# Kernel tuning notes

Hardware: AMD Instinct MI355X
Metric: run time of the kernel (lower is better)

## Reference

```python
import jax, jax.numpy as jnp
import numpy as np


def setup_inputs() -> dict:
    key = jax.random.key(0)
    k1, k2, k3, k4 = jax.random.split(key, 4)
    B, T, D, HS = 4, 2048, 1024, 64
    x = jax.random.normal(k1, (B, T, D), dtype=jnp.float32)
    # nn.Linear(d_model, head_size, bias=False) weights: (head_size, d_model)
    s = 1.0 / np.sqrt(D)
    Wk = jax.random.normal(k2, (HS, D), dtype=jnp.float32) * s
    Wq = jax.random.normal(k3, (HS, D), dtype=jnp.float32) * s
    Wv = jax.random.normal(k4, (HS, D), dtype=jnp.float32) * s
    return {"x": x, "Wk": Wk, "Wq": Wq, "Wv": Wv}


def reference(x, Wk, Wq, Wv):
    # x: [B, T, D]; W*: [HS, D]
    B, T, D = x.shape
    HS = Wk.shape[0]
    k = jnp.einsum('btd,hd->bth', x, Wk)  # [B, T, HS]
    q = jnp.einsum('btd,hd->bth', x, Wq)
    v = jnp.einsum('btd,hd->bth', x, Wv)
    # FAITHFUL to source bug: scores / hs**(-0.5) == scores * sqrt(hs)
    scale = jnp.asarray(np.sqrt(HS), dtype=x.dtype)
    scores = jnp.einsum('bqh,bkh->bqk', q, k) * scale  # [B, T, T]
    causal = jnp.tril(jnp.ones((T, T), dtype=bool))
    scores = jnp.where(causal, scores, jnp.asarray(-jnp.inf, dtype=scores.dtype))
    att = jax.nn.softmax(scores, axis=-1)  # dropout p=0.0 -> identity
    out = jnp.einsum('bqk,bkh->bqh', att, v)  # [B, T, HS]
    return out
```

## Files before the change

### kernel.cpp

```cpp
#include <hip/hip_runtime.h>

#define TSEQ 2048
#define DDIM 1024
#define HSZ  64
#define NB   4
#define NROWS (NB * TSEQ)

typedef short bf16x8 __attribute__((ext_vector_type(8)));
typedef short s16x4  __attribute__((ext_vector_type(4)));
typedef float f32x4  __attribute__((ext_vector_type(4)));
typedef unsigned int u32;
typedef unsigned int u32x4 __attribute__((ext_vector_type(4)));

#define MFMA16(a, b, c) __builtin_amdgcn_mfma_f32_16x16x32_bf16((a), (b), (c), 0, 0, 0)

__device__ inline void split_rn(float f, short& hi, short& lo) {
    u32 u = __builtin_bit_cast(u32, f);
    u32 rr = (u + 0x7fffu + ((u >> 16) & 1u)) & 0xffff0000u;
    hi = (short)(rr >> 16);
    float fh = __builtin_bit_cast(float, rr);
    float fl = f - fh;
    lo = (short)(__builtin_bit_cast(u32, fl) >> 16);
}

__device__ inline void gload_lds16(const void* g, void* l) {
    __builtin_amdgcn_global_load_lds((const __attribute__((address_space(1))) void*)g,
                                     (__attribute__((address_space(3))) void*)l, 16, 0, 0);
}

__global__ __launch_bounds__(256) void wsplit_kernel(
    const float* __restrict__ Wk, const float* __restrict__ Wq, const float* __restrict__ Wv,
    short* __restrict__ wbhi, short* __restrict__ wblo)
{
    int i = blockIdx.x * 256 + threadIdx.x;
    int off = i << 2;
    int which = off >> 16;
    int loc = off & 65535;
    const float* src = (which == 0) ? Wk : (which == 1) ? Wq : Wv;
    float4 v = *(const float4*)(src + loc);
    int row = off >> 10;
    int k = off & 1023;
    int kd = (k & ~63) | ((k & 63) ^ ((row & 7) << 3));
    int dst = (row << 10) | kd;
    short h0,h1,h2,h3, l0,l1,l2,l3;
    split_rn(v.x, h0, l0); split_rn(v.y, h1, l1);
    split_rn(v.z, h2, l2); split_rn(v.w, h3, l3);
    *(s16x4*)(wbhi + dst) = (s16x4){h0,h1,h2,h3};
    *(s16x4*)(wblo + dst) = (s16x4){l0,l1,l2,l3};
}

__global__ __launch_bounds__(512) void proj_mfma(
    const float* __restrict__ x,
    const short* __restrict__ wbhi, const short* __restrict__ wblo,
    short* __restrict__ khi, short* __restrict__ klo,
    short* __restrict__ qhi, short* __restrict__ qlo,
    short* __restrict__ vthi, short* __restrict__ vtlo)
{
    __shared__ __align__(16) short xhi[32][72], xlo[32][72];
    __shared__ __align__(16) short whi[192 * 64], wlo[192 * 64];

    const int tid  = threadIdx.x;
    const int w    = tid >> 6;
    const int lane = tid & 63;
    const int g    = lane >> 4;
    const int c    = lane & 15;
    const int rowoff = (w & 1) * 16;
    const int colgrp = w >> 1;
    const long rb  = (long)blockIdx.x * 32;

    f32x4 acc[3];
    acc[0] = 0; acc[1] = 0; acc[2] = 0;

    for (int k0 = 0; k0 < DDIM; k0 += 64) {
        {
            int row = tid >> 4, c4 = (tid & 15) << 2;
            float4 xv = *(const float4*)(x + (rb + row) * DDIM + k0 + c4);
            short h0,h1,h2,h3, l0,l1,l2,l3;
            split_rn(xv.x, h0, l0); split_rn(xv.y, h1, l1);
            split_rn(xv.z, h2, l2); split_rn(xv.w, h3, l3);
            *(s16x4*)&xhi[row][c4] = (s16x4){h0,h1,h2,h3};
            *(s16x4*)&xlo[row][c4] = (s16x4){l0,l1,l2,l3};
        }
        #pragma unroll
        for (int u = 0; u < 3; ++u) {
            int hchunk = w * 3 + u;
            int sidx = hchunk * 512 + lane * 8;
            int trow = sidx >> 6, tk = sidx & 63;
            gload_lds16(wbhi + trow * DDIM + k0 + tk, whi + hchunk * 512);
            gload_lds16(wblo + trow * DDIM + k0 + tk, wlo + hchunk * 512);
        }
        __syncthreads();

        #pragma unroll
        for (int kk = 0; kk < 2; ++kk) {
            bf16x8 ah = *(const bf16x8*)&xhi[rowoff + c][kk*32 + 8*g];
            bf16x8 al = *(const bf16x8*)&xlo[rowoff + c][kk*32 + 8*g];
            #pragma unroll
            for (int t = 0; t < 3; ++t) {
                int wr = colgrp * 48 + t * 16 + c;
                int koff = (kk*32 + 8*g) ^ ((wr & 7) << 3);
                bf16x8 bh = *(const bf16x8*)&whi[wr * 64 + koff];
                bf16x8 bl = *(const bf16x8*)&wlo[wr * 64 + koff];
                acc[t] = MFMA16(al, bh, acc[t]);
                acc[t] = MFMA16(ah, bl, acc[t]);
                acc[t] = MFMA16(ah, bh, acc[t]);
            }
        }
        __syncthreads();
    }

    __syncthreads();
    short (*vtrh)[36] = (short(*)[36])(&xhi[0][0]);
    short (*vtrl)[36] = (short(*)[36])(&xlo[0][0]);
    const int batch = (int)(rb >> 11);
    const int t0 = (int)(rb & 2047);
    #pragma unroll
    for (int t = 0; t < 3; ++t) {
        int col16 = colgrp * 48 + t * 16;
        int mode = col16 >> 6;
        int lcol = col16 - (mode << 6) + c;
        if (mode < 2) {
            short* oh = mode ? qhi : khi;
            short* ol = mode ? qlo : klo;
            const float sc = mode ? 8.0f : 1.0f;
            #pragma unroll
            for (int r = 0; r < 4; ++r) {
                long row = rb + rowoff + 4*g + r;
                short h, lo2; split_rn(acc[t][r] * sc, h, lo2);
                oh[row * HSZ + lcol] = h;
                ol[row * HSZ + lcol] = lo2;
            }
        } else {
            #pragma unroll
            for (int r = 0; r < 4; ++r) {
                short h, lo2; split_rn(acc[t][r], h, lo2);
                vtrh[lcol][rowoff + 4*g + r] = h;
                vtrl[lcol][rowoff + 4*g + r] = lo2;
            }
        }
    }
    __syncthreads();
    {
        int d = tid >> 3, t4 = (tid & 7) << 2;
        long gofs = ((long)(batch * HSZ + d)) * TSEQ + t0 + t4;
        *(s16x4*)(vthi + gofs) = *(const s16x4*)&vtrh[d][t4];
        *(s16x4*)(vtlo + gofs) = *(const s16x4*)&vtrl[d][t4];
    }
}

__global__ __launch_bounds__(512, 4) void attn_mfma(
    const short* __restrict__ qhi, const short* __restrict__ qlo,
    const short* __restrict__ khi, const short* __restrict__ klo,
    const short* __restrict__ vthi, const short* __restrict__ vtlo,
    float* __restrict__ out)
{
    __shared__ __align__(16) u32  pbuf[8][16][68];
    __shared__ float obuf[7][16][68];
    __shared__ float mlbuf[8][16][2];

    const int tid  = threadIdx.x;
    const int w    = tid >> 6;
    const int lane = tid & 63;
    const int g    = lane >> 4;
    const int c    = lane & 15;

    const int bid   = blockIdx.x;
    const int work  = ((bid & 7) << 6) | (bid >> 3);
    const int batch = work >> 7;
    const int rank  = work & 127;
    const int tile  = (rank < 64) ? (127 - 2*rank) : (126 - 2*(rank - 64));
    const int qb0   = tile << 4;
    const long bb   = (long)batch * TSEQ;

    bf16x8 qh[2], ql[2];
    {
        const long qofs = (bb + qb0 + c) * HSZ;
        #pragma unroll
        for (int kk = 0; kk < 2; ++kk) {
            qh[kk] = *(const bf16x8*)(qhi + qofs + kk*32 + 8*g);
            ql[kk] = *(const bf16x8*)(qlo + qofs + kk*32 + 8*g);
        }
    }

    f32x4 oacc[4];
    #pragma unroll
    for (int dt = 0; dt < 4; ++dt) oacc[dt] = 0;
    float m = -1e30f, l = 0.0f;

    const int lastkey = qb0 + 15;
    if (64 * w <= lastkey) {
        const int nsteps = ((lastkey - 64 * w) >> 9) + 1;
        for (int s = 0; s < nsteps; ++s) {
            const int jb = (s << 9) + (w << 6);
            f32x4 sa[4];
            sa[0] = 0; sa[1] = 0; sa[2] = 0; sa[3] = 0;
            #pragma unroll
            for (int kk = 0; kk < 2; ++kk) {
                bf16x8 kb_h[4], kb_l[4];
                #pragma unroll
                for (int t = 0; t < 4; ++t) {
                    const long kofs = (bb + jb + t*16 + c) * HSZ + kk*32 + 8*g;
                    kb_h[t] = *(const bf16x8*)(khi + kofs);
                    kb_l[t] = *(const bf16x8*)(klo + kofs);
                }
                #pragma unroll
                for (int t = 0; t < 4; ++t) {
                    sa[t] = MFMA16(kb_h[t], ql[kk], sa[t]);
                    sa[t] = MFMA16(kb_l[t], qh[kk], sa[t]);
                    sa[t] = MFMA16(kb_h[t], qh[kk], sa[t]);
                }
            }
            if (jb + 63 > qb0) {
                #pragma unroll
                for (int t = 0; t < 4; ++t) {
                    const int kb0 = jb + t*16 + 4*g;
                    #pragma unroll
                    for (int r = 0; r < 4; ++r)
                        if (kb0 + r > qb0 + c) sa[t][r] = -1e30f;
                }
            }
            float mx = sa[0][0];
            #pragma unroll
            for (int t = 0; t < 4; ++t)
                #pragma unroll
                for (int r = 0; r < 4; ++r) mx = fmaxf(mx, sa[t][r]);
            mx = fmaxf(mx, __shfl_xor(mx, 16));
            mx = fmaxf(mx, __shfl_xor(mx, 32));
            const float mn = fmaxf(m, mx);
            float rs = 0.0f;
            #pragma unroll
            for (int t = 0; t < 4; ++t) {
                #pragma unroll
                for (int r = 0; r < 4; ++r) {
                    float p = __expf(sa[t][r] - mn);
                    rs += p;
                    short h, lo2; split_rn(p, h, lo2);
                    pbuf[w][c][t*16 + 4*g + r] =
                        (u32)(unsigned short)h | ((u32)(unsigned short)lo2 << 16);
                }
            }
            rs += __shfl_xor(rs, 16);
            rs += __shfl_xor(rs, 32);
            const float fs = __expf(m - mn);
            l = l * fs + rs;
            m = mn;
            float fr[4];
            #pragma unroll
            for (int r = 0; r < 4; ++r) fr[r] = __shfl(fs, (g << 4) + 4*g + r);
            #pragma unroll
            for (int dt = 0; dt < 4; ++dt) {
                oacc[dt][0] *= fr[0]; oacc[dt][1] *= fr[1];
                oacc[dt][2] *= fr[2]; oacc[dt][3] *= fr[3];
            }
            #pragma unroll
            for (int kk = 0; kk < 2; ++kk) {
                u32x4 pw0 = *(const u32x4*)&pbuf[w][c][kk*32 + 8*g];
                u32x4 pw1 = *(const u32x4*)&pbuf[w][c][kk*32 + 8*g + 4];
                u32x4 th, tl;
                th[0] = (pw0[0] & 0xffffu) | (pw0[1] << 16);
                tl[0] = (pw0[0] >> 16)    | (pw0[1] & 0xffff0000u);
                th[1] = (pw0[2] & 0xffffu) | (pw0[3] << 16);
                tl[1] = (pw0[2] >> 16)    | (pw0[3] & 0xffff0000u);
                th[2] = (pw1[0] & 0xffffu) | (pw1[1] << 16);
                tl[2] = (pw1[0] >> 16)    | (pw1[1] & 0xffff0000u);
                th[3] = (pw1[2] & 0xffffu) | (pw1[3] << 16);
                tl[3] = (pw1[2] >> 16)    | (pw1[3] & 0xffff0000u);
                bf16x8 pah = __builtin_bit_cast(bf16x8, th);
                bf16x8 pal = __builtin_bit_cast(bf16x8, tl);
                bf16x8 vb_h[4], vb_l[4];
                #pragma unroll
                for (int dt = 0; dt < 4; ++dt) {
                    const long vofs = ((long)(batch * HSZ + dt*16 + c)) * TSEQ + jb + kk*32 + 8*g;
                    vb_h[dt] = *(const bf16x8*)(vthi + vofs);
                    vb_l[dt] = *(const bf16x8*)(vtlo + vofs);
                }
                #pragma unroll
                for (int dt = 0; dt < 4; ++dt) {
                    oacc[dt] = MFMA16(pal, vb_h[dt], oacc[dt]);
                    oacc[dt] = MFMA16(pah, vb_l[dt], oacc[dt]);
                    oacc[dt] = MFMA16(pah, vb_h[dt], oacc[dt]);
                }
            }
        }
    }

    if (lane < 16) { mlbuf[w][lane][0] = m; mlbuf[w][lane][1] = l; }
    if (w > 0) {
        #pragma unroll
        for (int dt = 0; dt < 4; ++dt)
            #pragma unroll
            for (int r = 0; r < 4; ++r)
                obuf[w-1][4*g + r][dt*16 + c] = oacc[dt][r];
    }
    __syncthreads();
    if (w == 0) {
        #pragma unroll
        for (int r = 0; r < 4; ++r) {
            const int row = 4*g + r;
            float ms = mlbuf[0][row][0];
            #pragma unroll
            for (int wv = 1; wv < 8; ++wv) ms = fmaxf(ms, mlbuf[wv][row][0]);
            float ls = 0.0f; float fw[8];
            #pragma unroll
            for (int wv = 0; wv < 8; ++wv) {
                fw[wv] = __expf(mlbuf[wv][row][0] - ms);
                ls += mlbuf[wv][row][1] * fw[wv];
            }
            const float linv = 1.0f / ls;
            #pragma unroll
            for (int dt = 0; dt < 4; ++dt) {
                float val = oacc[dt][r] * fw[0];
                #pragma unroll
                for (int wv = 1; wv < 8; ++wv) val += obuf[wv-1][row][dt*16 + c] * fw[wv];
                out[(bb + qb0 + row) * HSZ + dt*16 + c] = val * linv;
            }
        }
    }
}

extern "C" void kernel_launch(void* const* d_in, const int* in_sizes, int n_in,
                              void* d_out, int out_size, void* d_ws, size_t ws_size,
                              hipStream_t stream) {
    const float* x  = (const float*)d_in[0];
    const float* Wk = (const float*)d_in[1];
    const float* Wq = (const float*)d_in[2];
    const float* Wv = (const float*)d_in[3];
    float* out = (float*)d_out;

    short* ws = (short*)d_ws;
    const size_t SEG = (size_t)NROWS * HSZ;
    short* khi  = ws;
    short* klo  = ws + SEG;
    short* qhi  = ws + 2*SEG;
    short* qlo  = ws + 3*SEG;
    short* vthi = ws + 4*SEG;
    short* vtlo = ws + 5*SEG;
    short* wbhi = ws + 6*SEG;
    short* wblo = wbhi + 3*HSZ*DDIM;

    wsplit_kernel<<<192, 256, 0, stream>>>(Wk, Wq, Wv, wbhi, wblo);
    proj_mfma<<<256, 512, 0, stream>>>(x, wbhi, wblo, khi, klo, qhi, qlo, vthi, vtlo);
    attn_mfma<<<512, 512, 0, stream>>>(qhi, qlo, khi, klo, vthi, vtlo, out);
}
```

Baseline: 148.8 us.

## Process two query tiles per attention block and drop LDS staging in projection

The attention kernel now gives each block 32 query rows (two 16-row tiles), so every K/V fragment loaded from global memory feeds twice as many MFMAs. The grid is halved and launch bounds drop to 2 blocks per CU to leave room for the larger register set, at some cost in occupancy and causal load balance. Separately, the projection kernel loads x and the split weights straight from global memory into registers and removes LDS staging, the swizzle and the barriers. This relies on caches for weight reuse across waves instead of explicit shared-memory sharing.

```diff
diff --git a/kernel.cpp b/kernel.cpp
--- a/kernel.cpp
+++ b/kernel.cpp
@@ -21,11 +21,6 @@
     float fh = __builtin_bit_cast(float, rr);
     float fl = f - fh;
     lo = (short)(__builtin_bit_cast(u32, fl) >> 16);
-}
-
-__device__ inline void gload_lds16(const void* g, void* l) {
-    __builtin_amdgcn_global_load_lds((const __attribute__((address_space(1))) void*)g,
-                                     (__attribute__((address_space(3))) void*)l, 16, 0, 0);
 }
 
 __global__ __launch_bounds__(256) void wsplit_kernel(
@@ -38,15 +33,11 @@
     int loc = off & 65535;
     const float* src = (which == 0) ? Wk : (which == 1) ? Wq : Wv;
     float4 v = *(const float4*)(src + loc);
-    int row = off >> 10;
-    int k = off & 1023;
-    int kd = (k & ~63) | ((k & 63) ^ ((row & 7) << 3));
-    int dst = (row << 10) | kd;
     short h0,h1,h2,h3, l0,l1,l2,l3;
     split_rn(v.x, h0, l0); split_rn(v.y, h1, l1);
     split_rn(v.z, h2, l2); split_rn(v.w, h3, l3);
-    *(s16x4*)(wbhi + dst) = (s16x4){h0,h1,h2,h3};
-    *(s16x4*)(wblo + dst) = (s16x4){l0,l1,l2,l3};
+    *(s16x4*)(wbhi + off) = (s16x4){h0,h1,h2,h3};
+    *(s16x4*)(wblo + off) = (s16x4){l0,l1,l2,l3};
 }
 
 __global__ __launch_bounds__(512) void proj_mfma(
@@ -56,8 +47,7 @@
     short* __restrict__ qhi, short* __restrict__ qlo,
     short* __restrict__ vthi, short* __restrict__ vtlo)
 {
-    __shared__ __align__(16) short xhi[32][72], xlo[32][72];
-    __shared__ __align__(16) short whi[192 * 64], wlo[192 * 64];
+    __shared__ __align__(16) short vtrh[64][36], vtrl[64][36];
 
     const int tid  = threadIdx.x;
     const int w    = tid >> 6;
@@ -71,47 +61,40 @@
     f32x4 acc[3];
     acc[0] = 0; acc[1] = 0; acc[2] = 0;
 
+    const float* xrow = x + (rb + rowoff + c) * DDIM;
+    const int wr0 = colgrp * 48 + c;
+
+    #pragma unroll 2
     for (int k0 = 0; k0 < DDIM; k0 += 64) {
-        {
-            int row = tid >> 4, c4 = (tid & 15) << 2;
-            float4 xv = *(const float4*)(x + (rb + row) * DDIM + k0 + c4);
-            short h0,h1,h2,h3, l0,l1,l2,l3;
-            split_rn(xv.x, h0, l0); split_rn(xv.y, h1, l1);
-            split_rn(xv.z, h2, l2); split_rn(xv.w, h3, l3);
-            *(s16x4*)&xhi[row][c4] = (s16x4){h0,h1,h2,h3};
-            *(s16x4*)&xlo[row][c4] = (s16x4){l0,l1,l2,l3};
-        }
-        #pragma unroll
-        for (int u = 0; u < 3; ++u) {
-            int hchunk = w * 3 + u;
-            int sidx = hchunk * 512 + lane * 8;
-            int trow = sidx >> 6, tk = sidx & 63;
-            gload_lds16(wbhi + trow * DDIM + k0 + tk, whi + hchunk * 512);
-            gload_lds16(wblo + trow * DDIM + k0 + tk, wlo + hchunk * 512);
-        }
-        __syncthreads();
-
         #pragma unroll
         for (int kk = 0; kk < 2; ++kk) {
-            bf16x8 ah = *(const bf16x8*)&xhi[rowoff + c][kk*32 + 8*g];
-            bf16x8 al = *(const bf16x8*)&xlo[rowoff + c][kk*32 + 8*g];
+            const int off = k0 + kk*32 + 8*g;
+            float4 xa = *(const float4*)(xrow + off);
+            float4 xb = *(const float4*)(xrow + off + 4);
+            bf16x8 ah, al;
+            {
+                short h, lo2;
+                split_rn(xa.x, h, lo2); ah[0]=h; al[0]=lo2;
+                split_rn(xa.y, h, lo2); ah[1]=h; al[1]=lo2;
+                split_rn(xa.z, h, lo2); ah[2]=h; al[2]=lo2;
+                split_rn(xa.w, h, lo2); ah[3]=h; al[3]=lo2;
+                split_rn(xb.x, h, lo2); ah[4]=h; al[4]=lo2;
+                split_rn(xb.y, h, lo2); ah[5]=h; al[5]=lo2;
+                split_rn(xb.z, h, lo2); ah[6]=h; al[6]=lo2;
+                split_rn(xb.w, h, lo2); ah[7]=h; al[7]=lo2;
+            }
             #pragma unroll
             for (int t = 0; t < 3; ++t) {
-                int wr = colgrp * 48 + t * 16 + c;
-                int koff = (kk*32 + 8*g) ^ ((wr & 7) << 3);
-                bf16x8 bh = *(const bf16x8*)&whi[wr * 64 + koff];
-                bf16x8 bl = *(const bf16x8*)&wlo[wr * 64 + koff];
+                const long wofs = (long)(wr0 + t*16) * DDIM + off;
+                bf16x8 bh = *(const bf16x8*)(wbhi + wofs);
+                bf16x8 bl = *(const bf16x8*)(wblo + wofs);
                 acc[t] = MFMA16(al, bh, acc[t]);
                 acc[t] = MFMA16(ah, bl, acc[t]);
                 acc[t] = MFMA16(ah, bh, acc[t]);
             }
         }
-        __syncthreads();
-    }
-
-    __syncthreads();
-    short (*vtrh)[36] = (short(*)[36])(&xhi[0][0]);
-    short (*vtrl)[36] = (short(*)[36])(&xlo[0][0]);
+    }
+
     const int batch = (int)(rb >> 11);
     const int t0 = (int)(rb & 2047);
     #pragma unroll
@@ -148,15 +131,15 @@
     }
 }
 
-__global__ __launch_bounds__(512, 4) void attn_mfma(
+__global__ __launch_bounds__(512, 2) void attn_mfma(
     const short* __restrict__ qhi, const short* __restrict__ qlo,
     const short* __restrict__ khi, const short* __restrict__ klo,
     const short* __restrict__ vthi, const short* __restrict__ vtlo,
     float* __restrict__ out)
 {
-    __shared__ __align__(16) u32  pbuf[8][16][68];
-    __shared__ float obuf[7][16][68];
-    __shared__ float mlbuf[8][16][2];
+    __shared__ __align__(16) u32 pbuf[8][2][16][68];
+    __shared__ float obuf[7][2][16][68];
+    __shared__ float mlbuf[8][2][16][2];
 
     const int tid  = threadIdx.x;
     const int w    = tid >> 6;
@@ -165,154 +148,190 @@
     const int c    = lane & 15;
 
     const int bid   = blockIdx.x;
-    const int work  = ((bid & 7) << 6) | (bid >> 3);
-    const int batch = work >> 7;
-    const int rank  = work & 127;
-    const int tile  = (rank < 64) ? (127 - 2*rank) : (126 - 2*(rank - 64));
-    const int qb0   = tile << 4;
+    const int u     = 63 - (bid >> 2);
+    const int batch = bid & 3;
+    const int qA0   = u << 5;
     const long bb   = (long)batch * TSEQ;
-
-    bf16x8 qh[2], ql[2];
-    {
-        const long qofs = (bb + qb0 + c) * HSZ;
+    const int lastkey = qA0 + 31;
+
+    bf16x8 qh[2][2], ql[2][2];
+    #pragma unroll
+    for (int tt = 0; tt < 2; ++tt) {
+        const long qofs = (bb + qA0 + tt*16 + c) * HSZ;
         #pragma unroll
         for (int kk = 0; kk < 2; ++kk) {
-            qh[kk] = *(const bf16x8*)(qhi + qofs + kk*32 + 8*g);
-            ql[kk] = *(const bf16x8*)(qlo + qofs + kk*32 + 8*g);
-        }
-    }
-
-    f32x4 oacc[4];
+            qh[tt][kk] = *(const bf16x8*)(qhi + qofs + kk*32 + 8*g);
+            ql[tt][kk] = *(const bf16x8*)(qlo + qofs + kk*32 + 8*g);
+        }
+    }
+
+    f32x4 oacc[2][4];
     #pragma unroll
-    for (int dt = 0; dt < 4; ++dt) oacc[dt] = 0;
-    float m = -1e30f, l = 0.0f;
-
-    const int lastkey = qb0 + 15;
+    for (int tt = 0; tt < 2; ++tt)
+        #pragma unroll
+        for (int dt = 0; dt < 4; ++dt) oacc[tt][dt] = 0;
+    float m[2] = {-1e30f, -1e30f}, l[2] = {0.0f, 0.0f};
+
     if (64 * w <= lastkey) {
         const int nsteps = ((lastkey - 64 * w) >> 9) + 1;
         for (int s = 0; s < nsteps; ++s) {
             const int jb = (s << 9) + (w << 6);
-            f32x4 sa[4];
-            sa[0] = 0; sa[1] = 0; sa[2] = 0; sa[3] = 0;
-            #pragma unroll
-            for (int kk = 0; kk < 2; ++kk) {
-                bf16x8 kb_h[4], kb_l[4];
+            bf16x8 kb_h[2][4], kb_l[2][4];
+            #pragma unroll
+            for (int kk = 0; kk < 2; ++kk)
                 #pragma unroll
                 for (int t = 0; t < 4; ++t) {
                     const long kofs = (bb + jb + t*16 + c) * HSZ + kk*32 + 8*g;
-                    kb_h[t] = *(const bf16x8*)(khi + kofs);
-                    kb_l[t] = *(const bf16x8*)(klo + kofs);
-                }
+                    kb_h[kk][t] = *(const bf16x8*)(khi + kofs);
+                    kb_l[kk][t] = *(const bf16x8*)(klo + kofs);
+                }
+            f32x4 sa[2][4];
+            #pragma unroll
+            for (int tt = 0; tt < 2; ++tt)
+                #pragma unroll
+                for (int t = 0; t < 4; ++t) sa[tt][t] = 0;
+            #pragma unroll
+            for (int kk = 0; kk < 2; ++kk)
                 #pragma unroll
                 for (int t = 0; t < 4; ++t) {
-                    sa[t] = MFMA16(kb_h[t], ql[kk], sa[t]);
-                    sa[t] = MFMA16(kb_l[t], qh[kk], sa[t]);
-                    sa[t] = MFMA16(kb_h[t], qh[kk], sa[t]);
-                }
-            }
-            if (jb + 63 > qb0) {
-                #pragma unroll
-                for (int t = 0; t < 4; ++t) {
-                    const int kb0 = jb + t*16 + 4*g;
-                    #pragma unroll
-                    for (int r = 0; r < 4; ++r)
-                        if (kb0 + r > qb0 + c) sa[t][r] = -1e30f;
-                }
-            }
-            float mx = sa[0][0];
-            #pragma unroll
-            for (int t = 0; t < 4; ++t)
-                #pragma unroll
-                for (int r = 0; r < 4; ++r) mx = fmaxf(mx, sa[t][r]);
-            mx = fmaxf(mx, __shfl_xor(mx, 16));
-            mx = fmaxf(mx, __shfl_xor(mx, 32));
-            const float mn = fmaxf(m, mx);
-            float rs = 0.0f;
-            #pragma unroll
-            for (int t = 0; t < 4; ++t) {
-                #pragma unroll
-                for (int r = 0; r < 4; ++r) {
-                    float p = __expf(sa[t][r] - mn);
-                    rs += p;
-                    short h, lo2; split_rn(p, h, lo2);
-                    pbuf[w][c][t*16 + 4*g + r] =
-                        (u32)(unsigned short)h | ((u32)(unsigned short)lo2 << 16);
-                }
-            }
-            rs += __shfl_xor(rs, 16);
-            rs += __shfl_xor(rs, 32);
-            const float fs = __expf(m - mn);
-            l = l * fs + rs;
-            m = mn;
-            float fr[4];
-            #pragma unroll
-            for (int r = 0; r < 4; ++r) fr[r] = __shfl(fs, (g << 4) + 4*g + r);
-            #pragma unroll
-            for (int dt = 0; dt < 4; ++dt) {
-                oacc[dt][0] *= fr[0]; oacc[dt][1] *= fr[1];
-                oacc[dt][2] *= fr[2]; oacc[dt][3] *= fr[3];
-            }
-            #pragma unroll
-            for (int kk = 0; kk < 2; ++kk) {
-                u32x4 pw0 = *(const u32x4*)&pbuf[w][c][kk*32 + 8*g];
-                u32x4 pw1 = *(const u32x4*)&pbuf[w][c][kk*32 + 8*g + 4];
-                u32x4 th, tl;
-                th[0] = (pw0[0] & 0xffffu) | (pw0[1] << 16);
-                tl[0] = (pw0[0] >> 16)    | (pw0[1] & 0xffff0000u);
-                th[1] = (pw0[2] & 0xffffu) | (pw0[3] << 16);
-                tl[1] = (pw0[2] >> 16)    | (pw0[3] & 0xffff0000u);
-                th[2] = (pw1[0] & 0xffffu) | (pw1[1] << 16);
-                tl[2] = (pw1[0] >> 16)    | (pw1[1] & 0xffff0000u);
-                th[3] = (pw1[2] & 0xffffu) | (pw1[3] << 16);
-                tl[3] = (pw1[2] >> 16)    | (pw1[3] & 0xffff0000u);
-                bf16x8 pah = __builtin_bit_cast(bf16x8, th);
-                bf16x8 pal = __builtin_bit_cast(bf16x8, tl);
-                bf16x8 vb_h[4], vb_l[4];
+                    #pragma unroll
+                    for (int tt = 0; tt < 2; ++tt) {
+                        sa[tt][t] = MFMA16(kb_h[kk][t], ql[tt][kk], sa[tt][t]);
+                        sa[tt][t] = MFMA16(kb_l[kk][t], qh[tt][kk], sa[tt][t]);
+                        sa[tt][t] = MFMA16(kb_h[kk][t], qh[tt][kk], sa[tt][t]);
+                    }
+                }
+            bf16x8 vb_h[2][4], vb_l[2][4];
+            #pragma unroll
+            for (int kk = 0; kk < 2; ++kk)
                 #pragma unroll
                 for (int dt = 0; dt < 4; ++dt) {
                     const long vofs = ((long)(batch * HSZ + dt*16 + c)) * TSEQ + jb + kk*32 + 8*g;
-                    vb_h[dt] = *(const bf16x8*)(vthi + vofs);
-                    vb_l[dt] = *(const bf16x8*)(vtlo + vofs);
-                }
+                    vb_h[kk][dt] = *(const bf16x8*)(vthi + vofs);
+                    vb_l[kk][dt] = *(const bf16x8*)(vtlo + vofs);
+                }
+            #pragma unroll
+            for (int tt = 0; tt < 2; ++tt) {
+                const int q0 = qA0 + tt*16;
+                if (jb + 63 > q0) {
+                    #pragma unroll
+                    for (int t = 0; t < 4; ++t) {
+                        const int kb0 = jb + t*16 + 4*g;
+                        #pragma unroll
+                        for (int r = 0; r < 4; ++r)
+                            if (kb0 + r > q0 + c) sa[tt][t][r] = -1e30f;
+                    }
+                }
+            }
+            #pragma unroll
+            for (int tt = 0; tt < 2; ++tt) {
+                float mx = sa[tt][0][0];
+                #pragma unroll
+                for (int t = 0; t < 4; ++t)
+                    #pragma unroll
+                    for (int r = 0; r < 4; ++r) mx = fmaxf(mx, sa[tt][t][r]);
+                mx = fmaxf(mx, __shfl_xor(mx, 16));
+                mx = fmaxf(mx, __shfl_xor(mx, 32));
+                const float mn = fmaxf(m[tt], mx);
+                float rs = 0.0f;
+                #pragma unroll
+                for (int t = 0; t < 4; ++t) {
+                    #pragma unroll
+                    for (int r = 0; r < 4; ++r) {
+                        float p = __expf(sa[tt][t][r] - mn);
+                        rs += p;
+                        short h, lo2; split_rn(p, h, lo2);
+                        pbuf[w][tt][c][t*16 + 4*g + r] =
+                            (u32)(unsigned short)h | ((u32)(unsigned short)lo2 << 16);
+                    }
+                }
+                rs += __shfl_xor(rs, 16);
+                rs += __shfl_xor(rs, 32);
+                const float fs = __expf(m[tt] - mn);
+                l[tt] = l[tt] * fs + rs;
+                m[tt] = mn;
+                float fr[4];
+                #pragma unroll
+                for (int r = 0; r < 4; ++r) fr[r] = __shfl(fs, 20*g + r);
                 #pragma unroll
                 for (int dt = 0; dt < 4; ++dt) {
-                    oacc[dt] = MFMA16(pal, vb_h[dt], oacc[dt]);
-                    oacc[dt] = MFMA16(pah, vb_l[dt], oacc[dt]);
-                    oacc[dt] = MFMA16(pah, vb_h[dt], oacc[dt]);
-                }
-            }
-        }
-    }
-
-    if (lane < 16) { mlbuf[w][lane][0] = m; mlbuf[w][lane][1] = l; }
+                    oacc[tt][dt][0] *= fr[0]; oacc[tt][dt][1] *= fr[1];
+                    oacc[tt][dt][2] *= fr[2]; oacc[tt][dt][3] *= fr[3];
+                }
+            }
+            #pragma unroll
+            for (int kk = 0; kk < 2; ++kk) {
+                bf16x8 pah[2], pal[2];
+                #pragma unroll
+                for (int tt = 0; tt < 2; ++tt) {
+                    u32x4 pw0 = *(const u32x4*)&pbuf[w][tt][c][kk*32 + 8*g];
+                    u32x4 pw1 = *(const u32x4*)&pbuf[w][tt][c][kk*32 + 8*g + 4];
+                    u32x4 th, tl;
+                    th[0] = (pw0[0] & 0xffffu) | (pw0[1] << 16);
+                    tl[0] = (pw0[0] >> 16)    | (pw0[1] & 0xffff0000u);
+                    th[1] = (pw0[2] & 0xffffu) | (pw0[3] << 16);
+                    tl[1] = (pw0[2] >> 16)    | (pw0[3] & 0xffff0000u);
+                    th[2] = (pw1[0] & 0xffffu) | (pw1[1] << 16);
+                    tl[2] = (pw1[0] >> 16)    | (pw1[1] & 0xffff0000u);
+                    th[3] = (pw1[2] & 0xffffu) | (pw1[3] << 16);
+                    tl[3] = (pw1[2] >> 16)    | (pw1[3] & 0xffff0000u);
+                    pah[tt] = __builtin_bit_cast(bf16x8, th);
+                    pal[tt] = __builtin_bit_cast(bf16x8, tl);
+                }
+                #pragma unroll
+                for (int dt = 0; dt < 4; ++dt) {
+                    #pragma unroll
+                    for (int tt = 0; tt < 2; ++tt) {
+                        oacc[tt][dt] = MFMA16(pal[tt], vb_h[kk][dt], oacc[tt][dt]);
+                        oacc[tt][dt] = MFMA16(pah[tt], vb_l[kk][dt], oacc[tt][dt]);
+                        oacc[tt][dt] = MFMA16(pah[tt], vb_h[kk][dt], oacc[tt][dt]);
+                    }
+                }
+            }
+        }
+    }
+
+    if (lane < 16) {
+        #pragma unroll
+        for (int tt = 0; tt < 2; ++tt) {
+            mlbuf[w][tt][lane][0] = m[tt];
+            mlbuf[w][tt][lane][1] = l[tt];
+        }
+    }
     if (w > 0) {
         #pragma unroll
-        for (int dt = 0; dt < 4; ++dt)
-            #pragma unroll
-            for (int r = 0; r < 4; ++r)
-                obuf[w-1][4*g + r][dt*16 + c] = oacc[dt][r];
+        for (int tt = 0; tt < 2; ++tt)
+            #pragma unroll
+            for (int dt = 0; dt < 4; ++dt)
+                #pragma unroll
+                for (int r = 0; r < 4; ++r)
+                    obuf[w-1][tt][4*g + r][dt*16 + c] = oacc[tt][dt][r];
     }
     __syncthreads();
     if (w == 0) {
         #pragma unroll
-        for (int r = 0; r < 4; ++r) {
-            const int row = 4*g + r;
-            float ms = mlbuf[0][row][0];
-            #pragma unroll
-            for (int wv = 1; wv < 8; ++wv) ms = fmaxf(ms, mlbuf[wv][row][0]);
-            float ls = 0.0f; float fw[8];
-            #pragma unroll
-            for (int wv = 0; wv < 8; ++wv) {
-                fw[wv] = __expf(mlbuf[wv][row][0] - ms);
-                ls += mlbuf[wv][row][1] * fw[wv];
-            }
-            const float linv = 1.0f / ls;
-            #pragma unroll
-            for (int dt = 0; dt < 4; ++dt) {
-                float val = oacc[dt][r] * fw[0];
-                #pragma unroll
-                for (int wv = 1; wv < 8; ++wv) val += obuf[wv-1][row][dt*16 + c] * fw[wv];
-                out[(bb + qb0 + row) * HSZ + dt*16 + c] = val * linv;
+        for (int tt = 0; tt < 2; ++tt) {
+            #pragma unroll
+            for (int r = 0; r < 4; ++r) {
+                const int row = 4*g + r;
+                float ms = mlbuf[0][tt][row][0];
+                #pragma unroll
+                for (int wv = 1; wv < 8; ++wv) ms = fmaxf(ms, mlbuf[wv][tt][row][0]);
+                float ls = 0.0f; float fw[8];
+                #pragma unroll
+                for (int wv = 0; wv < 8; ++wv) {
+                    fw[wv] = __expf(mlbuf[wv][tt][row][0] - ms);
+                    ls += mlbuf[wv][tt][row][1] * fw[wv];
+                }
+                const float linv = 1.0f / ls;
+                #pragma unroll
+                for (int dt = 0; dt < 4; ++dt) {
+                    float val = oacc[tt][dt][r] * fw[0];
+                    #pragma unroll
+                    for (int wv = 1; wv < 8; ++wv)
+                        val += obuf[wv-1][tt][row][dt*16 + c] * fw[wv];
+                    out[(bb + qA0 + tt*16 + row) * HSZ + dt*16 + c] = val * linv;
+                }
             }
         }
     }
@@ -340,5 +359,5 @@
 
     wsplit_kernel<<<192, 256, 0, stream>>>(Wk, Wq, Wv, wbhi, wblo);
     proj_mfma<<<256, 512, 0, stream>>>(x, wbhi, wblo, khi, klo, qhi, qlo, vthi, vtlo);
-    attn_mfma<<<512, 512, 0, stream>>>(qhi, qlo, khi, klo, vthi, vtlo, out);
-}
+    attn_mfma<<<256, 512, 0, stream>>>(qhi, qlo, khi, klo, vthi, vtlo, out);
+}
```

After: 168.8 us. +13.5%, slower.

## Drop low-precision split for P and V, restructure projection grid and merge

Applied to the files above, without the earlier changes.

The P·V product now uses a single bf16 MFMA per tile: the low-order bf16 halves of P and V are dropped, so V's low buffer is no longer written. The projection kernel is reorganised into a 2D grid with one block per (64-row tile, K/Q/V mode), using plain vector loads in place of global_load_lds and no weight swizzle. The attention kernel also prefetches V before the softmax, skips the accumulator rescale when no row max changes, adds s_setprio around MFMA bursts, and merges per-wave partial outputs with a tree reduction. Together these cut MFMA count, memory traffic and serial merge work, at the cost of lower precision in the P·V product.

```diff
diff --git a/kernel.cpp b/kernel.cpp
--- a/kernel.cpp
+++ b/kernel.cpp
@@ -10,7 +10,6 @@
 typedef short s16x4  __attribute__((ext_vector_type(4)));
 typedef float f32x4  __attribute__((ext_vector_type(4)));
 typedef unsigned int u32;
-typedef unsigned int u32x4 __attribute__((ext_vector_type(4)));
 
 #define MFMA16(a, b, c) __builtin_amdgcn_mfma_f32_16x16x32_bf16((a), (b), (c), 0, 0, 0)
 
@@ -22,10 +21,9 @@
     float fl = f - fh;
     lo = (short)(__builtin_bit_cast(u32, fl) >> 16);
 }
-
-__device__ inline void gload_lds16(const void* g, void* l) {
-    __builtin_amdgcn_global_load_lds((const __attribute__((address_space(1))) void*)g,
-                                     (__attribute__((address_space(3))) void*)l, 16, 0, 0);
+__device__ inline short bf16rn(float f) {
+    u32 u = __builtin_bit_cast(u32, f);
+    return (short)((u + 0x7fffu + ((u >> 16) & 1u)) >> 16);
 }
 
 __global__ __launch_bounds__(256) void wsplit_kernel(
@@ -38,124 +36,125 @@
     int loc = off & 65535;
     const float* src = (which == 0) ? Wk : (which == 1) ? Wq : Wv;
     float4 v = *(const float4*)(src + loc);
-    int row = off >> 10;
-    int k = off & 1023;
-    int kd = (k & ~63) | ((k & 63) ^ ((row & 7) << 3));
-    int dst = (row << 10) | kd;
     short h0,h1,h2,h3, l0,l1,l2,l3;
     split_rn(v.x, h0, l0); split_rn(v.y, h1, l1);
     split_rn(v.z, h2, l2); split_rn(v.w, h3, l3);
-    *(s16x4*)(wbhi + dst) = (s16x4){h0,h1,h2,h3};
-    *(s16x4*)(wblo + dst) = (s16x4){l0,l1,l2,l3};
-}
-
-__global__ __launch_bounds__(512) void proj_mfma(
+    *(s16x4*)(wbhi + off) = (s16x4){h0,h1,h2,h3};
+    *(s16x4*)(wblo + off) = (s16x4){l0,l1,l2,l3};
+}
+
+__global__ __launch_bounds__(256, 3) void proj_mfma(
     const float* __restrict__ x,
     const short* __restrict__ wbhi, const short* __restrict__ wblo,
     short* __restrict__ khi, short* __restrict__ klo,
     short* __restrict__ qhi, short* __restrict__ qlo,
-    short* __restrict__ vthi, short* __restrict__ vtlo)
+    short* __restrict__ vthi)
 {
-    __shared__ __align__(16) short xhi[32][72], xlo[32][72];
-    __shared__ __align__(16) short whi[192 * 64], wlo[192 * 64];
+    __shared__ __align__(16) short xh[64][88], xl[64][88];
+    __shared__ __align__(16) short wh[64][88], wl[64][88];
 
     const int tid  = threadIdx.x;
-    const int w    = tid >> 6;
+    const int wv   = tid >> 6;
     const int lane = tid & 63;
     const int g    = lane >> 4;
     const int c    = lane & 15;
-    const int rowoff = (w & 1) * 16;
-    const int colgrp = w >> 1;
-    const long rb  = (long)blockIdx.x * 32;
-
-    f32x4 acc[3];
-    acc[0] = 0; acc[1] = 0; acc[2] = 0;
+    const int mode = blockIdx.y;
+    const long rb  = (long)blockIdx.x * 64;
+
+    const int srow = tid >> 2;
+    const int skq  = (tid & 3) << 4;
+    const float* xp  = x + (rb + srow) * DDIM + skq;
+    const short* whp = wbhi + mode * (HSZ * DDIM) + srow * DDIM + skq;
+    const short* wlp = wblo + mode * (HSZ * DDIM) + srow * DDIM + skq;
+
+    f32x4 acc[4];
+    acc[0] = 0; acc[1] = 0; acc[2] = 0; acc[3] = 0;
 
     for (int k0 = 0; k0 < DDIM; k0 += 64) {
         {
-            int row = tid >> 4, c4 = (tid & 15) << 2;
-            float4 xv = *(const float4*)(x + (rb + row) * DDIM + k0 + c4);
-            short h0,h1,h2,h3, l0,l1,l2,l3;
-            split_rn(xv.x, h0, l0); split_rn(xv.y, h1, l1);
-            split_rn(xv.z, h2, l2); split_rn(xv.w, h3, l3);
-            *(s16x4*)&xhi[row][c4] = (s16x4){h0,h1,h2,h3};
-            *(s16x4*)&xlo[row][c4] = (s16x4){l0,l1,l2,l3};
-        }
-        #pragma unroll
-        for (int u = 0; u < 3; ++u) {
-            int hchunk = w * 3 + u;
-            int sidx = hchunk * 512 + lane * 8;
-            int trow = sidx >> 6, tk = sidx & 63;
-            gload_lds16(wbhi + trow * DDIM + k0 + tk, whi + hchunk * 512);
-            gload_lds16(wblo + trow * DDIM + k0 + tk, wlo + hchunk * 512);
+            float4 f0 = *(const float4*)(xp + k0);
+            float4 f1 = *(const float4*)(xp + k0 + 4);
+            float4 f2 = *(const float4*)(xp + k0 + 8);
+            float4 f3 = *(const float4*)(xp + k0 + 12);
+            float fv[16] = {f0.x,f0.y,f0.z,f0.w, f1.x,f1.y,f1.z,f1.w,
+                            f2.x,f2.y,f2.z,f2.w, f3.x,f3.y,f3.z,f3.w};
+            short hh[16], ll[16];
+            #pragma unroll
+            for (int j = 0; j < 16; ++j) split_rn(fv[j], hh[j], ll[j]);
+            #pragma unroll
+            for (int u = 0; u < 2; ++u) {
+                *(bf16x8*)&xh[srow][skq + 8*u] = *(bf16x8*)&hh[8*u];
+                *(bf16x8*)&xl[srow][skq + 8*u] = *(bf16x8*)&ll[8*u];
+            }
+        }
+        {
+            bf16x8 a0 = *(const bf16x8*)(whp + k0);
+            bf16x8 a1 = *(const bf16x8*)(whp + k0 + 8);
+            bf16x8 b0 = *(const bf16x8*)(wlp + k0);
+            bf16x8 b1 = *(const bf16x8*)(wlp + k0 + 8);
+            *(bf16x8*)&wh[srow][skq]     = a0;
+            *(bf16x8*)&wh[srow][skq + 8] = a1;
+            *(bf16x8*)&wl[srow][skq]     = b0;
+            *(bf16x8*)&wl[srow][skq + 8] = b1;
         }
         __syncthreads();
 
         #pragma unroll
         for (int kk = 0; kk < 2; ++kk) {
-            bf16x8 ah = *(const bf16x8*)&xhi[rowoff + c][kk*32 + 8*g];
-            bf16x8 al = *(const bf16x8*)&xlo[rowoff + c][kk*32 + 8*g];
-            #pragma unroll
-            for (int t = 0; t < 3; ++t) {
-                int wr = colgrp * 48 + t * 16 + c;
-                int koff = (kk*32 + 8*g) ^ ((wr & 7) << 3);
-                bf16x8 bh = *(const bf16x8*)&whi[wr * 64 + koff];
-                bf16x8 bl = *(const bf16x8*)&wlo[wr * 64 + koff];
-                acc[t] = MFMA16(al, bh, acc[t]);
-                acc[t] = MFMA16(ah, bl, acc[t]);
-                acc[t] = MFMA16(ah, bh, acc[t]);
-            }
+            bf16x8 ah = *(const bf16x8*)&xh[16*wv + c][kk*32 + 8*g];
+            bf16x8 al = *(const bf16x8*)&xl[16*wv + c][kk*32 + 8*g];
+            __builtin_amdgcn_s_setprio(1);
+            #pragma unroll
+            for (int ct = 0; ct < 4; ++ct) {
+                bf16x8 bh = *(const bf16x8*)&wh[ct*16 + c][kk*32 + 8*g];
+                bf16x8 bl = *(const bf16x8*)&wl[ct*16 + c][kk*32 + 8*g];
+                acc[ct] = MFMA16(al, bh, acc[ct]);
+                acc[ct] = MFMA16(ah, bl, acc[ct]);
+                acc[ct] = MFMA16(ah, bh, acc[ct]);
+            }
+            __builtin_amdgcn_s_setprio(0);
         }
         __syncthreads();
     }
 
-    __syncthreads();
-    short (*vtrh)[36] = (short(*)[36])(&xhi[0][0]);
-    short (*vtrl)[36] = (short(*)[36])(&xlo[0][0]);
     const int batch = (int)(rb >> 11);
-    const int t0 = (int)(rb & 2047);
-    #pragma unroll
-    for (int t = 0; t < 3; ++t) {
-        int col16 = colgrp * 48 + t * 16;
-        int mode = col16 >> 6;
-        int lcol = col16 - (mode << 6) + c;
-        if (mode < 2) {
-            short* oh = mode ? qhi : khi;
-            short* ol = mode ? qlo : klo;
-            const float sc = mode ? 8.0f : 1.0f;
+    const int t0    = (int)(rb & 2047);
+    if (mode < 2) {
+        short* oh = mode ? qhi : khi;
+        short* ol = mode ? qlo : klo;
+        const float sc = mode ? 8.0f : 1.0f;
+        #pragma unroll
+        for (int ct = 0; ct < 4; ++ct) {
             #pragma unroll
             for (int r = 0; r < 4; ++r) {
-                long row = rb + rowoff + 4*g + r;
-                short h, lo2; split_rn(acc[t][r] * sc, h, lo2);
-                oh[row * HSZ + lcol] = h;
-                ol[row * HSZ + lcol] = lo2;
-            }
-        } else {
-            #pragma unroll
-            for (int r = 0; r < 4; ++r) {
-                short h, lo2; split_rn(acc[t][r], h, lo2);
-                vtrh[lcol][rowoff + 4*g + r] = h;
-                vtrl[lcol][rowoff + 4*g + r] = lo2;
-            }
-        }
-    }
-    __syncthreads();
-    {
-        int d = tid >> 3, t4 = (tid & 7) << 2;
-        long gofs = ((long)(batch * HSZ + d)) * TSEQ + t0 + t4;
-        *(s16x4*)(vthi + gofs) = *(const s16x4*)&vtrh[d][t4];
-        *(s16x4*)(vtlo + gofs) = *(const s16x4*)&vtrl[d][t4];
+                long row = rb + 16*wv + 4*g + r;
+                short h, lo2; split_rn(acc[ct][r] * sc, h, lo2);
+                oh[row * HSZ + ct*16 + c] = h;
+                ol[row * HSZ + ct*16 + c] = lo2;
+            }
+        }
+    } else {
+        #pragma unroll
+        for (int ct = 0; ct < 4; ++ct)
+            #pragma unroll
+            for (int r = 0; r < 4; ++r)
+                wh[ct*16 + c][16*wv + 4*g + r] = bf16rn(acc[ct][r]);
+        __syncthreads();
+        const int d = tid >> 2, t16 = (tid & 3) << 4;
+        long gofs = ((long)(batch * HSZ + d)) * TSEQ + t0 + t16;
+        *(bf16x8*)(vthi + gofs)     = *(const bf16x8*)&wh[d][t16];
+        *(bf16x8*)(vthi + gofs + 8) = *(const bf16x8*)&wh[d][t16 + 8];
     }
 }
 
 __global__ __launch_bounds__(512, 4) void attn_mfma(
     const short* __restrict__ qhi, const short* __restrict__ qlo,
     const short* __restrict__ khi, const short* __restrict__ klo,
-    const short* __restrict__ vthi, const short* __restrict__ vtlo,
+    const short* __restrict__ vthi,
     float* __restrict__ out)
 {
-    __shared__ __align__(16) u32  pbuf[8][16][68];
-    __shared__ float obuf[7][16][68];
+    __shared__ __align__(16) short pbuf[8][16][88];
+    __shared__ float obuf[4][16][68];
     __shared__ float mlbuf[8][16][2];
 
     const int tid  = threadIdx.x;
@@ -171,6 +170,7 @@
     const int tile  = (rank < 64) ? (127 - 2*rank) : (126 - 2*(rank - 64));
     const int qb0   = tile << 4;
     const long bb   = (long)batch * TSEQ;
+    const int lastkey = qb0 + 15;
 
     bf16x8 qh[2], ql[2];
     {
@@ -187,7 +187,6 @@
     for (int dt = 0; dt < 4; ++dt) oacc[dt] = 0;
     float m = -1e30f, l = 0.0f;
 
-    const int lastkey = qb0 + 15;
     if (64 * w <= lastkey) {
         const int nsteps = ((lastkey - 64 * w) >> 9) + 1;
         for (int s = 0; s < nsteps; ++s) {
@@ -203,13 +202,23 @@
                     kb_h[t] = *(const bf16x8*)(khi + kofs);
                     kb_l[t] = *(const bf16x8*)(klo + kofs);
                 }
+                __builtin_amdgcn_s_setprio(1);
                 #pragma unroll
                 for (int t = 0; t < 4; ++t) {
                     sa[t] = MFMA16(kb_h[t], ql[kk], sa[t]);
                     sa[t] = MFMA16(kb_l[t], qh[kk], sa[t]);
                     sa[t] = MFMA16(kb_h[t], qh[kk], sa[t]);
                 }
-            }
+                __builtin_amdgcn_s_setprio(0);
+            }
+            bf16x8 vb[2][4];
+            #pragma unroll
+            for (int kk = 0; kk < 2; ++kk)
+                #pragma unroll
+                for (int dt = 0; dt < 4; ++dt) {
+                    const long vofs = ((long)(batch * HSZ + dt*16 + c)) * TSEQ + jb + kk*32 + 8*g;
+                    vb[kk][dt] = *(const bf16x8*)(vthi + vofs);
+                }
             if (jb + 63 > qb0) {
                 #pragma unroll
                 for (int t = 0; t < 4; ++t) {
@@ -226,95 +235,113 @@
                 for (int r = 0; r < 4; ++r) mx = fmaxf(mx, sa[t][r]);
             mx = fmaxf(mx, __shfl_xor(mx, 16));
             mx = fmaxf(mx, __shfl_xor(mx, 32));
-            const float mn = fmaxf(m, mx);
+            const float mold = m;
+            const float mn = fmaxf(mold, mx);
             float rs = 0.0f;
             #pragma unroll
             for (int t = 0; t < 4; ++t) {
-                #pragma unroll
-                for (int r = 0; r < 4; ++r) {
-                    float p = __expf(sa[t][r] - mn);
-                    rs += p;
-                    short h, lo2; split_rn(p, h, lo2);
-                    pbuf[w][c][t*16 + 4*g + r] =
-                        (u32)(unsigned short)h | ((u32)(unsigned short)lo2 << 16);
-                }
+                float p0 = __expf(sa[t][0] - mn);
+                float p1 = __expf(sa[t][1] - mn);
+                float p2 = __expf(sa[t][2] - mn);
+                float p3 = __expf(sa[t][3] - mn);
+                rs += (p0 + p1) + (p2 + p3);
+                u32 w0 = (u32)(unsigned short)bf16rn(p0) | ((u32)(unsigned short)bf16rn(p1) << 16);
+                u32 w1 = (u32)(unsigned short)bf16rn(p2) | ((u32)(unsigned short)bf16rn(p3) << 16);
+                *(u32*)&pbuf[w][c][t*16 + 4*g]     = w0;
+                *(u32*)&pbuf[w][c][t*16 + 4*g + 2] = w1;
             }
             rs += __shfl_xor(rs, 16);
             rs += __shfl_xor(rs, 32);
-            const float fs = __expf(m - mn);
+            const float fs = __expf(mold - mn);
             l = l * fs + rs;
             m = mn;
-            float fr[4];
-            #pragma unroll
-            for (int r = 0; r < 4; ++r) fr[r] = __shfl(fs, (g << 4) + 4*g + r);
-            #pragma unroll
-            for (int dt = 0; dt < 4; ++dt) {
-                oacc[dt][0] *= fr[0]; oacc[dt][1] *= fr[1];
-                oacc[dt][2] *= fr[2]; oacc[dt][3] *= fr[3];
+            if (__any(mn > mold)) {
+                float fr[4];
+                #pragma unroll
+                for (int r = 0; r < 4; ++r) fr[r] = __shfl(fs, 16*g + 4*g + r);
+                #pragma unroll
+                for (int dt = 0; dt < 4; ++dt) {
+                    oacc[dt][0] *= fr[0]; oacc[dt][1] *= fr[1];
+                    oacc[dt][2] *= fr[2]; oacc[dt][3] *= fr[3];
+                }
             }
             #pragma unroll
             for (int kk = 0; kk < 2; ++kk) {
-                u32x4 pw0 = *(const u32x4*)&pbuf[w][c][kk*32 + 8*g];
-                u32x4 pw1 = *(const u32x4*)&pbuf[w][c][kk*32 + 8*g + 4];
-                u32x4 th, tl;
-                th[0] = (pw0[0] & 0xffffu) | (pw0[1] << 16);
-                tl[0] = (pw0[0] >> 16)    | (pw0[1] & 0xffff0000u);
-                th[1] = (pw0[2] & 0xffffu) | (pw0[3] << 16);
-                tl[1] = (pw0[2] >> 16)    | (pw0[3] & 0xffff0000u);
-                th[2] = (pw1[0] & 0xffffu) | (pw1[1] << 16);
-                tl[2] = (pw1[0] >> 16)    | (pw1[1] & 0xffff0000u);
-                th[3] = (pw1[2] & 0xffffu) | (pw1[3] << 16);
-                tl[3] = (pw1[2] >> 16)    | (pw1[3] & 0xffff0000u);
-                bf16x8 pah = __builtin_bit_cast(bf16x8, th);
-                bf16x8 pal = __builtin_bit_cast(bf16x8, tl);
-                bf16x8 vb_h[4], vb_l[4];
-                #pragma unroll
-                for (int dt = 0; dt < 4; ++dt) {
-                    const long vofs = ((long)(batch * HSZ + dt*16 + c)) * TSEQ + jb + kk*32 + 8*g;
-                    vb_h[dt] = *(const bf16x8*)(vthi + vofs);
-                    vb_l[dt] = *(const bf16x8*)(vtlo + vofs);
-                }
-                #pragma unroll
-                for (int dt = 0; dt < 4; ++dt) {
-                    oacc[dt] = MFMA16(pal, vb_h[dt], oacc[dt]);
-                    oacc[dt] = MFMA16(pah, vb_l[dt], oacc[dt]);
-                    oacc[dt] = MFMA16(pah, vb_h[dt], oacc[dt]);
-                }
+                bf16x8 pa = *(const bf16x8*)&pbuf[w][c][kk*32 + 8*g];
+                __builtin_amdgcn_s_setprio(1);
+                #pragma unroll
+                for (int dt = 0; dt < 4; ++dt)
+                    oacc[dt] = MFMA16(pa, vb[kk][dt], oacc[dt]);
+                __builtin_amdgcn_s_setprio(0);
             }
         }
     }
 
     if (lane < 16) { mlbuf[w][lane][0] = m; mlbuf[w][lane][1] = l; }
-    if (w > 0) {
-        #pragma unroll
-        for (int dt = 0; dt < 4; ++dt)
-            #pragma unroll
-            for (int r = 0; r < 4; ++r)
-                obuf[w-1][4*g + r][dt*16 + c] = oacc[dt][r];
+    __syncthreads();
+    float fw_[4], linv_[4];
+    #pragma unroll
+    for (int r = 0; r < 4; ++r) {
+        const int row = 4*g + r;
+        float ms = mlbuf[0][row][0];
+        #pragma unroll
+        for (int wv = 1; wv < 8; ++wv) ms = fmaxf(ms, mlbuf[wv][row][0]);
+        float ls = 0.0f;
+        #pragma unroll
+        for (int wv = 0; wv < 8; ++wv)
+            ls += __expf(mlbuf[wv][row][0] - ms) * mlbuf[wv][row][1];
+        fw_[r] = __expf(mlbuf[w][row][0] - ms);
+        linv_[r] = 1.0f / ls;
+    }
+    #pragma unroll
+    for (int dt = 0; dt < 4; ++dt) {
+        oacc[dt][0] *= fw_[0]; oacc[dt][1] *= fw_[1];
+        oacc[dt][2] *= fw_[2]; oacc[dt][3] *= fw_[3];
+    }
+    if (w >= 4)
+        #pragma unroll
+        for (int dt = 0; dt < 4; ++dt)
+            #pragma unroll
+            for (int r = 0; r < 4; ++r)
+                obuf[w-4][4*g + r][dt*16 + c] = oacc[dt][r];
+    __syncthreads();
+    if (w < 4)
+        #pragma unroll
+        for (int dt = 0; dt < 4; ++dt)
+            #pragma unroll
+            for (int r = 0; r < 4; ++r)
+                oacc[dt][r] += obuf[w][4*g + r][dt*16 + c];
+    if (w == 2 || w == 3)
+        #pragma unroll
+        for (int dt = 0; dt < 4; ++dt)
+            #pragma unroll
+            for (int r = 0; r < 4; ++r)
+                obuf[w][4*g + r][dt*16 + c] = oacc[dt][r];
+    __syncthreads();
+    if (w == 0)
+        #pragma unroll
+        for (int dt = 0; dt < 4; ++dt)
+            #pragma unroll
+            for (int r = 0; r < 4; ++r)
+                oacc[dt][r] += obuf[2][4*g + r][dt*16 + c];
+    if (w == 1) {
+        #pragma unroll
+        for (int dt = 0; dt < 4; ++dt)
+            #pragma unroll
+            for (int r = 0; r < 4; ++r) {
+                oacc[dt][r] += obuf[3][4*g + r][dt*16 + c];
+                obuf[1][4*g + r][dt*16 + c] = oacc[dt][r];
+            }
     }
     __syncthreads();
     if (w == 0) {
         #pragma unroll
-        for (int r = 0; r < 4; ++r) {
-            const int row = 4*g + r;
-            float ms = mlbuf[0][row][0];
-            #pragma unroll
-            for (int wv = 1; wv < 8; ++wv) ms = fmaxf(ms, mlbuf[wv][row][0]);
-            float ls = 0.0f; float fw[8];
-            #pragma unroll
-            for (int wv = 0; wv < 8; ++wv) {
-                fw[wv] = __expf(mlbuf[wv][row][0] - ms);
-                ls += mlbuf[wv][row][1] * fw[wv];
-            }
-            const float linv = 1.0f / ls;
-            #pragma unroll
-            for (int dt = 0; dt < 4; ++dt) {
-                float val = oacc[dt][r] * fw[0];
-                #pragma unroll
-                for (int wv = 1; wv < 8; ++wv) val += obuf[wv-1][row][dt*16 + c] * fw[wv];
-                out[(bb + qb0 + row) * HSZ + dt*16 + c] = val * linv;
-            }
-        }
+        for (int dt = 0; dt < 4; ++dt)
+            #pragma unroll
+            for (int r = 0; r < 4; ++r) {
+                float val = (oacc[dt][r] + obuf[1][4*g + r][dt*16 + c]) * linv_[r];
+                out[(bb + qb0 + 4*g + r) * HSZ + dt*16 + c] = val;
+            }
     }
 }
 
@@ -334,11 +361,11 @@
     short* qhi  = ws + 2*SEG;
     short* qlo  = ws + 3*SEG;
     short* vthi = ws + 4*SEG;
-    short* vtlo = ws + 5*SEG;
-    short* wbhi = ws + 6*SEG;
+    short* wbhi = ws + 5*SEG;
     short* wblo = wbhi + 3*HSZ*DDIM;
 
     wsplit_kernel<<<192, 256, 0, stream>>>(Wk, Wq, Wv, wbhi, wblo);
-    proj_mfma<<<256, 512, 0, stream>>>(x, wbhi, wblo, khi, klo, qhi, qlo, vthi, vtlo);
-    attn_mfma<<<512, 512, 0, stream>>>(qhi, qlo, khi, klo, vthi, vtlo, out);
-}
+    proj_mfma<<<dim3(128, 3), 256, 0, stream>>>(x, wbhi, wblo,
+                                                khi, klo, qhi, qlo, vthi);
+    attn_mfma<<<512, 512, 0, stream>>>(qhi, qlo, khi, klo, vthi, out);
+}
```

Result: faster. 135.6 us (-8.9%).
